# Optimization experiments

Hardware: AMD Instinct MI355X
Metric: run time of the kernel (lower is better)

The kernel has to match this reference:

```python
import jax, jax.numpy as jnp
import numpy as np

TOP_K = 2
B, T, D, H, E = 4, 2048, 1024, 2048, 8


def setup_inputs() -> dict:
    key = jax.random.key(0)
    ks = jax.random.split(key, 5)
    x = jax.random.normal(ks[0], (B, T, D), dtype=jnp.float32)
    # router: nn.Linear(dim, n_exp, bias=True) -> weight [E, D], bias [E]
    router_w = jax.random.normal(ks[1], (E, D), dtype=jnp.float32) * (D ** -0.5)
    router_b = jnp.zeros((E,), dtype=jnp.float32)
    # experts stacked: gate/up weight [E, H, D], down weight [E, D, H] (torch Linear is [out, in])
    w_gate = jax.random.normal(ks[2], (E, H, D), dtype=jnp.float32) * (D ** -0.5)
    w_up = jax.random.normal(ks[3], (E, H, D), dtype=jnp.float32) * (D ** -0.5)
    w_down = jax.random.normal(ks[4], (E, D, H), dtype=jnp.float32) * (H ** -0.5)
    return {"x": x, "router_w": router_w, "router_b": router_b,
            "w_gate": w_gate, "w_up": w_up, "w_down": w_down}


def reference(x, router_w, router_b, w_gate, w_up, w_down):
    b, t, d = x.shape
    n_exp = router_w.shape[0]
    flat = x.reshape(-1, d)                                  # [N, D]
    logits = flat @ router_w.T + router_b                    # [N, E]
    probs = jax.nn.softmax(logits, axis=-1)
    top_vals, top_idx = jax.lax.top_k(probs, TOP_K)          # [N, K]
    top_vals = top_vals / (jnp.sum(top_vals, axis=-1, keepdims=True) + 1e-9)
    # dense combine weights [N, E]: scatter normalized top-k probs to expert slots
    comb = jnp.sum(jax.nn.one_hot(top_idx, n_exp, dtype=flat.dtype) * top_vals[..., None], axis=1)
    # run every expert on every token (jit-friendly dense form of gather/scatter loop)
    g = jnp.einsum('nd,ehd->enh', flat, w_gate)              # [E, N, H]
    u = jnp.einsum('nd,ehd->enh', flat, w_up)
    h = jax.nn.silu(g) * u                                   # SwiGLU
    e_out = jnp.einsum('enh,edh->end', h, w_down)            # [E, N, D]
    out = jnp.einsum('ne,end->nd', comb, e_out)              # weighted combine
    return out.reshape(b, t, d)
```

## Files before the change

kernel.cpp:

```cpp
#include <hip/hip_runtime.h>
#include <hip/hip_bf16.h>
#include <stdint.h>


#define N_TOK 8192
#define D_DIM 1024
#define H_DIM 2048
#define N_EXP 8
#define N_ASSIGN (N_TOK * 2)
#define BM 128
#define BN 128
#define BK 64

typedef __attribute__((ext_vector_type(8))) short short8;
typedef __attribute__((ext_vector_type(4))) float f32x4;

__device__ __forceinline__ unsigned short f2bf(float f) {
  union { float f; unsigned int u; } v; v.f = f;
  unsigned int r = v.u + 0x7fffu + ((v.u >> 16) & 1u);
  return (unsigned short)(r >> 16);
}
__device__ __forceinline__ float bf2f(unsigned short u) {
  union { float f; unsigned int u; } v; v.u = ((unsigned int)u) << 16; return v.f;
}
__device__ __forceinline__ short8 pack8(float4 a, float4 b) {
  short8 o;
  o[0] = (short)f2bf(a.x); o[1] = (short)f2bf(a.y);
  o[2] = (short)f2bf(a.z); o[3] = (short)f2bf(a.w);
  o[4] = (short)f2bf(b.x); o[5] = (short)f2bf(b.y);
  o[6] = (short)f2bf(b.z); o[7] = (short)f2bf(b.w);
  return o;
}
__device__ __forceinline__ void gload_lds16(const void* g, void* l) {
  __builtin_amdgcn_global_load_lds((const __attribute__((address_space(1))) void*)g,
                                   (__attribute__((address_space(3))) void*)l, 16, 0, 0);
}

__global__ __launch_bounds__(256) void router_prep_kernel(
    const float* __restrict__ x, const float* __restrict__ rw,
    const float* __restrict__ rb,
    const float* __restrict__ wg, const float* __restrict__ wu,
    unsigned short* __restrict__ xb, unsigned short* __restrict__ wgu,
    int2* __restrict__ tiidx, float2* __restrict__ tiw) {
  int b = blockIdx.x;
  int tid = threadIdx.x;
  if (b >= 2048) {
    int idx = b - 2048;
    int up = idx >> 13;
    size_t i = (((size_t)(idx & 8191)) * 256 + tid) * 8;
    const float* src = up ? wu : wg;
    float4 a = *(const float4*)(src + i);
    float4 c = *(const float4*)(src + i + 4);
    int j = (int)(i >> 10);
    int e = j >> 11;
    int jj = j & (H_DIM - 1);
    int n = ((jj >> 4) << 5) + (up ? 16 : 0) + (jj & 15);
    size_t di = (((size_t)(e << 12) + n) << 10) + (i & 1023);
    *(short8*)(wgu + di) = pack8(a, c);
    return;
  }

  __shared__ float sw[N_EXP][D_DIM];
  for (int i = tid * 4; i < N_EXP * D_DIM; i += 1024)
    *(float4*)&sw[0][i] = *(const float4*)(rw + i);
  __syncthreads();

  int wave = tid >> 6, lane = tid & 63;
  int t = b * 4 + wave;
  const float2* xr = (const float2*)(x + (size_t)t * D_DIM);
  float2 xs[8];
#pragma unroll
  for (int j = 0; j < 8; j++) xs[j] = xr[lane + 64 * j];
  unsigned int* xbo = (unsigned int*)(xb + (size_t)t * D_DIM);
#pragma unroll
  for (int j = 0; j < 8; j++) {
    unsigned int pk = ((unsigned int)f2bf(xs[j].y) << 16) | (unsigned int)f2bf(xs[j].x);
    xbo[lane + 64 * j] = pk;
  }

  float logit[N_EXP];
#pragma unroll
  for (int e = 0; e < N_EXP; e++) {
    float acc = 0.f;
    const float2* swe = (const float2*)sw[e];
#pragma unroll
    for (int j = 0; j < 8; j++) {
      float2 w2 = swe[lane + 64 * j];
      acc += xs[j].x * w2.x + xs[j].y * w2.y;
    }
#pragma unroll
    for (int off = 32; off; off >>= 1) acc += __shfl_xor(acc, off);
    logit[e] = acc + rb[e];
  }
  if (lane == 0) {
    float m = logit[0];
#pragma unroll
    for (int e = 1; e < N_EXP; e++) m = fmaxf(m, logit[e]);
    float p[N_EXP], S = 0.f;
#pragma unroll
    for (int e = 0; e < N_EXP; e++) { p[e] = expf(logit[e] - m); S += p[e]; }
#pragma unroll
    for (int e = 0; e < N_EXP; e++) p[e] /= S;
    int i1 = 0; float v1 = p[0];
#pragma unroll
    for (int e = 1; e < N_EXP; e++) if (p[e] > v1) { v1 = p[e]; i1 = e; }
    int i2 = -1; float v2 = -1.f;
#pragma unroll
    for (int e = 0; e < N_EXP; e++) if (e != i1 && p[e] > v2) { v2 = p[e]; i2 = e; }
    float inv = 1.f / (v1 + v2 + 1e-9f);
    tiidx[t] = make_int2(i1, i2);
    tiw[t] = make_float2(v1 * inv, v2 * inv);
  }
}

__global__ __launch_bounds__(256) void plan_kernel(
    const int2* __restrict__ tiidx, int* __restrict__ cnt,
    int* __restrict__ off, int* __restrict__ assign, int2* __restrict__ trows) {
  __shared__ int sh[256][N_EXP + 1];
  __shared__ int soff[N_EXP];
  int tid = threadIdx.x;
  int t0 = tid * 32;

#pragma unroll
  for (int e = 0; e < N_EXP; e++) sh[tid][e] = 0;
  for (int i = 0; i < 32; i++) {
    int2 te = tiidx[t0 + i];
    sh[tid][te.x]++;
    sh[tid][te.y]++;
  }
  int oc[N_EXP];
#pragma unroll
  for (int e = 0; e < N_EXP; e++) oc[e] = sh[tid][e];
  __syncthreads();

  for (int s = 1; s < 256; s <<= 1) {
    int v[N_EXP];
#pragma unroll
    for (int e = 0; e < N_EXP; e++) v[e] = (tid >= s) ? sh[tid - s][e] : 0;
    __syncthreads();
#pragma unroll
    for (int e = 0; e < N_EXP; e++) sh[tid][e] += v[e];
    __syncthreads();
  }

  int ex[N_EXP];
#pragma unroll
  for (int e = 0; e < N_EXP; e++) ex[e] = sh[tid][e] - oc[e];
  if (tid == 0) {
    int a = 0;
    for (int e = 0; e < N_EXP; e++) {
      int tot = sh[255][e];
      soff[e] = a; off[e] = a; cnt[e] = tot; a += tot;
    }
    off[N_EXP] = a;
  }
  __syncthreads();
#pragma unroll
  for (int e = 0; e < N_EXP; e++) sh[tid][e] = ex[e];
  __syncthreads();

  for (int i = 0; i < 32; i++) {
    int t = t0 + i;
    int2 te = tiidx[t];
    int r1 = soff[te.x] + sh[tid][te.x]++;
    int r2 = soff[te.y] + sh[tid][te.y]++;
    assign[r1] = t;
    assign[r2] = t;
    trows[t] = make_int2(r1, r2);
  }
}

__global__ __launch_bounds__(256) void gemm_gateup(
    const unsigned short* __restrict__ xb,
    const unsigned short* __restrict__ wgu,
    const float* __restrict__ wd,
    unsigned short* __restrict__ wdb,
    const int* __restrict__ cnt, const int* __restrict__ off,
    const int* __restrict__ assign,
    unsigned short* __restrict__ hbuf) {
  int tid = threadIdx.x;
  if (blockIdx.z == 8) {
    size_t b0 = ((size_t)(blockIdx.x + 32 * blockIdx.y)) * 8192;
#pragma unroll
    for (int it = 0; it < 4; it++) {
      size_t i = b0 + ((size_t)it * 256 + tid) * 8;
      float4 a = *(const float4*)(wd + i);
      float4 c = *(const float4*)(wd + i + 4);
      *(short8*)(wdb + i) = pack8(a, c);
    }
    return;
  }
  int e = blockIdx.z;
  int nrows = cnt[e];
  int row0 = blockIdx.y * BM;
  if (row0 >= nrows) return;
  int col0 = blockIdx.x * BN;
  int base = off[e];

  __shared__ unsigned short sA[2][BM][BK];
  __shared__ unsigned short sB[2][BN][BK];

  int srow = tid >> 3;
  int dst8 = (tid & 7) * 8;
  int src8 = ((tid & 7) ^ (srow & 7)) * 8;

  const unsigned short* asrc[4];
  const unsigned short* bsrc[4];
#pragma unroll
  for (int i = 0; i < 4; i++) {
    int r = row0 + srow + 32 * i;
    int tok = (r < nrows) ? assign[base + r] : assign[base];
    asrc[i] = xb + (size_t)tok * D_DIM + src8;
    int wrow = (e << 12) + col0 + srow + 32 * i;
    bsrc[i] = wgu + (size_t)wrow * D_DIM + src8;
  }

  int wr = (tid >> 7) & 1, wc = (tid >> 6) & 1;
  int lane = tid & 63;
  int fr = lane & 15;
  int fk = (lane >> 4) * 8;
  int rx = (fr & 7) * 8;

  f32x4 acc[4][4];
#pragma unroll
  for (int a = 0; a < 4; a++)
#pragma unroll
    for (int b = 0; b < 4; b++) acc[a][b] = (f32x4){0.f, 0.f, 0.f, 0.f};

#define STAGE(bf, k0)                                                       \
  _Pragma("unroll")                                                         \
  for (int i = 0; i < 4; i++) {                                             \
    gload_lds16(asrc[i] + (k0), &sA[bf][srow + 32 * i][dst8]);              \
    gload_lds16(bsrc[i] + (k0), &sB[bf][srow + 32 * i][dst8]);              \
  }
#define COMPUTE(bf)                                                         \
  _Pragma("unroll")                                                         \
  for (int ks = 0; ks < 2; ks++) {                                          \
    short8 af[4], bq[4];                                                    \
    int c = (ks * 32 + fk) ^ rx;                                            \
    _Pragma("unroll")                                                       \
    for (int mb = 0; mb < 4; mb++)                                          \
      af[mb] = *(const short8*)&sA[bf][wr * 64 + mb * 16 + fr][c];          \
    _Pragma("unroll")                                                       \
    for (int nb = 0; nb < 4; nb++)                                          \
      bq[nb] = *(const short8*)&sB[bf][wc * 64 + nb * 16 + fr][c];          \
    _Pragma("unroll")                                                       \
    for (int mb = 0; mb < 4; mb++)                                          \
      _Pragma("unroll")                                                     \
      for (int nb = 0; nb < 4; nb++)                                        \
        acc[mb][nb] = __builtin_amdgcn_mfma_f32_16x16x32_bf16(              \
            af[mb], bq[nb], acc[mb][nb], 0, 0, 0);                          \
  }

  STAGE(0, 0);
  __syncthreads();
  for (int k0 = 0; k0 < D_DIM - 128; k0 += 128) {
    STAGE(1, k0 + 64);  COMPUTE(0); __syncthreads();
    STAGE(0, k0 + 128); COMPUTE(1); __syncthreads();
  }
  STAGE(1, D_DIM - 64); COMPUTE(0); __syncthreads();
  COMPUTE(1);
#undef STAGE
#undef COMPUTE

  int rowlim = nrows - row0;
#pragma unroll
  for (int mb = 0; mb < 4; mb++)
#pragma unroll
    for (int r = 0; r < 4; r++) {
      int lrow = wr * 64 + mb * 16 + (lane >> 4) * 4 + r;
      if (lrow < rowlim) {
        size_t hrow = (size_t)(base + row0 + lrow);
#pragma unroll
        for (int nbp = 0; nbp < 2; nbp++) {
          float g = acc[mb][2 * nbp][r], u = acc[mb][2 * nbp + 1][r];
          float hv = g / (1.f + __expf(-g)) * u;
          int hcol = (col0 >> 1) + wc * 32 + nbp * 16 + (lane & 15);
          hbuf[hrow * H_DIM + hcol] = f2bf(hv);
        }
      }
    }
}

__global__ __launch_bounds__(256) void gemm_down(
    const unsigned short* __restrict__ hbuf,
    const unsigned short* __restrict__ wd,
    const int* __restrict__ cnt, const int* __restrict__ off,
    unsigned short* __restrict__ eo) {
  int e = blockIdx.z;
  int nrows = cnt[e];
  int row0 = blockIdx.y * BM;
  if (row0 >= nrows) return;
  int col0 = blockIdx.x * BN;
  int base = off[e];

  __shared__ unsigned short sA[2][BM][BK];
  __shared__ unsigned short sB[2][BN][BK];

  int tid = threadIdx.x;
  int srow = tid >> 3;
  int dst8 = (tid & 7) * 8;
  int src8 = ((tid & 7) ^ (srow & 7)) * 8;

  const unsigned short* asrc[4];
  const unsigned short* bsrc[4];
#pragma unroll
  for (int i = 0; i < 4; i++) {
    int r = row0 + srow + 32 * i;
    int hrow = base + ((r < nrows) ? r : 0);
    asrc[i] = hbuf + (size_t)hrow * H_DIM + src8;
    int wrow = e * D_DIM + col0 + srow + 32 * i;
    bsrc[i] = wd + (size_t)wrow * H_DIM + src8;
  }

  int wr = (tid >> 7) & 1, wc = (tid >> 6) & 1;
  int lane = tid & 63;
  int fr = lane & 15;
  int fk = (lane >> 4) * 8;
  int rx = (fr & 7) * 8;

  f32x4 acc[4][4];
#pragma unroll
  for (int a = 0; a < 4; a++)
#pragma unroll
    for (int b = 0; b < 4; b++) acc[a][b] = (f32x4){0.f, 0.f, 0.f, 0.f};

#define STAGE(bf, k0)                                                       \
  _Pragma("unroll")                                                         \
  for (int i = 0; i < 4; i++) {                                             \
    gload_lds16(asrc[i] + (k0), &sA[bf][srow + 32 * i][dst8]);              \
    gload_lds16(bsrc[i] + (k0), &sB[bf][srow + 32 * i][dst8]);              \
  }
#define COMPUTE(bf)                                                         \
  _Pragma("unroll")                                                         \
  for (int ks = 0; ks < 2; ks++) {                                          \
    short8 af[4], bq[4];                                                    \
    int c = (ks * 32 + fk) ^ rx;                                            \
    _Pragma("unroll")                                                       \
    for (int mb = 0; mb < 4; mb++)                                          \
      af[mb] = *(const short8*)&sA[bf][wr * 64 + mb * 16 + fr][c];          \
    _Pragma("unroll")                                                       \
    for (int nb = 0; nb < 4; nb++)                                          \
      bq[nb] = *(const short8*)&sB[bf][wc * 64 + nb * 16 + fr][c];          \
    _Pragma("unroll")                                                       \
    for (int mb = 0; mb < 4; mb++)                                          \
      _Pragma("unroll")                                                     \
      for (int nb = 0; nb < 4; nb++)                                        \
        acc[mb][nb] = __builtin_amdgcn_mfma_f32_16x16x32_bf16(              \
            af[mb], bq[nb], acc[mb][nb], 0, 0, 0);                          \
  }

  STAGE(0, 0);
  __syncthreads();
  for (int k0 = 0; k0 < H_DIM - 128; k0 += 128) {
    STAGE(1, k0 + 64);  COMPUTE(0); __syncthreads();
    STAGE(0, k0 + 128); COMPUTE(1); __syncthreads();
  }
  STAGE(1, H_DIM - 64); COMPUTE(0); __syncthreads();
  COMPUTE(1);
#undef STAGE
#undef COMPUTE

  int rowlim = nrows - row0;
#pragma unroll
  for (int mb = 0; mb < 4; mb++)
#pragma unroll
    for (int r = 0; r < 4; r++) {
      int lrow = wr * 64 + mb * 16 + (lane >> 4) * 4 + r;
      if (lrow < rowlim) {
        size_t orow = (size_t)(base + row0 + lrow);
#pragma unroll
        for (int nb = 0; nb < 4; nb++)
          eo[orow * D_DIM + col0 + wc * 64 + nb * 16 + (lane & 15)] = f2bf(acc[mb][nb][r]);
      }
    }
}

__global__ __launch_bounds__(256) void combine_kernel(
    const unsigned short* __restrict__ eo, const int2* __restrict__ trows,
    const float2* __restrict__ tiw, float* __restrict__ out) {
  int t = blockIdx.x * 2 + (threadIdx.x >> 7);
  int l = threadIdx.x & 127;
  int c = l * 8;
  int2 r = trows[t];
  float2 w = tiw[t];
  short8 a = *(const short8*)&eo[(size_t)r.x * D_DIM + c];
  short8 b = *(const short8*)&eo[(size_t)r.y * D_DIM + c];
  float4 o0, o1;
  o0.x = w.x * bf2f((unsigned short)a[0]) + w.y * bf2f((unsigned short)b[0]);
  o0.y = w.x * bf2f((unsigned short)a[1]) + w.y * bf2f((unsigned short)b[1]);
  o0.z = w.x * bf2f((unsigned short)a[2]) + w.y * bf2f((unsigned short)b[2]);
  o0.w = w.x * bf2f((unsigned short)a[3]) + w.y * bf2f((unsigned short)b[3]);
  o1.x = w.x * bf2f((unsigned short)a[4]) + w.y * bf2f((unsigned short)b[4]);
  o1.y = w.x * bf2f((unsigned short)a[5]) + w.y * bf2f((unsigned short)b[5]);
  o1.z = w.x * bf2f((unsigned short)a[6]) + w.y * bf2f((unsigned short)b[6]);
  o1.w = w.x * bf2f((unsigned short)a[7]) + w.y * bf2f((unsigned short)b[7]);
  *(float4*)&out[(size_t)t * D_DIM + c] = o0;
  *(float4*)&out[(size_t)t * D_DIM + c + 4] = o1;
}

extern "C" void kernel_launch(void* const* d_in, const int* in_sizes, int n_in,
                              void* d_out, int out_size, void* d_ws, size_t ws_size,
                              hipStream_t stream) {
  const float* x  = (const float*)d_in[0];
  const float* rw = (const float*)d_in[1];
  const float* rb = (const float*)d_in[2];
  const float* wg = (const float*)d_in[3];
  const float* wu = (const float*)d_in[4];
  const float* wd = (const float*)d_in[5];
  float* out = (float*)d_out;

  char* ws = (char*)d_ws;
  size_t o = 0;
  auto alloc = [&](size_t b) { char* p = ws + o; o += (b + 255) & ~(size_t)255; return p; };
  unsigned short* xb  = (unsigned short*)alloc((size_t)N_TOK * D_DIM * 2);
  unsigned short* wgu = (unsigned short*)alloc((size_t)N_EXP * 4096 * D_DIM * 2);
  unsigned short* wdb = (unsigned short*)alloc((size_t)N_EXP * D_DIM * H_DIM * 2);
  unsigned short* hb  = (unsigned short*)alloc((size_t)N_ASSIGN * H_DIM * 2);
  unsigned short* eob = (unsigned short*)alloc((size_t)N_ASSIGN * D_DIM * 2);
  int*    assign = (int*)alloc(N_ASSIGN * 4);
  int2*   tiidx  = (int2*)alloc(N_TOK * 8);
  float2* tiw    = (float2*)alloc(N_TOK * 8);
  int2*   trows  = (int2*)alloc(N_TOK * 8);
  int*    cnt    = (int*)alloc(64);
  int*    off    = (int*)alloc(64);

  router_prep_kernel<<<2048 + 16384, 256, 0, stream>>>(
      x, rw, rb, wg, wu, xb, wgu, tiidx, tiw);
  plan_kernel<<<1, 256, 0, stream>>>(tiidx, cnt, off, assign, trows);
  gemm_gateup<<<dim3(4096 / BN, N_TOK / BM, N_EXP + 1), 256, 0, stream>>>(
      xb, wgu, wd, wdb, cnt, off, assign, hb);
  gemm_down<<<dim3(D_DIM / BN, N_TOK / BM, N_EXP), 256, 0, stream>>>(
      hb, wdb, cnt, off, eob);
  combine_kernel<<<N_TOK / 2, 256, 0, stream>>>(eob, trows, tiw, out);
}
```

Before: 352.5 us.

## Enlarge gate/up GEMM tile to 256x256 with 512 threads and tighter pipeline

```diff
diff --git a/kernel.cpp b/kernel.cpp
--- a/kernel.cpp
+++ b/kernel.cpp
@@ -170,7 +170,7 @@
   }
 }
 
-__global__ __launch_bounds__(256) void gemm_gateup(
+__global__ __launch_bounds__(512, 2) void gemm_gateup(
     const unsigned short* __restrict__ xb,
     const unsigned short* __restrict__ wgu,
     const float* __restrict__ wd,
@@ -180,10 +180,10 @@
     unsigned short* __restrict__ hbuf) {
   int tid = threadIdx.x;
   if (blockIdx.z == 8) {
-    size_t b0 = ((size_t)(blockIdx.x + 32 * blockIdx.y)) * 8192;
-#pragma unroll
-    for (int it = 0; it < 4; it++) {
-      size_t i = b0 + ((size_t)it * 256 + tid) * 8;
+    size_t b0 = ((size_t)(blockIdx.x + 16 * blockIdx.y)) * 4096;
+#pragma unroll
+    for (int it = 0; it < 8; it++) {
+      size_t i = (b0 + (size_t)it * 512 + tid) * 8;
       float4 a = *(const float4*)(wd + i);
       float4 c = *(const float4*)(wd + i + 4);
       *(short8*)(wdb + i) = pack8(a, c);
@@ -192,13 +192,13 @@
   }
   int e = blockIdx.z;
   int nrows = cnt[e];
-  int row0 = blockIdx.y * BM;
+  int row0 = blockIdx.y * 256;
   if (row0 >= nrows) return;
-  int col0 = blockIdx.x * BN;
+  int col0 = blockIdx.x * 256;
   int base = off[e];
 
-  __shared__ unsigned short sA[2][BM][BK];
-  __shared__ unsigned short sB[2][BN][BK];
+  __shared__ unsigned short sA[2][256][BK];
+  __shared__ unsigned short sB[2][256][BK];
 
   int srow = tid >> 3;
   int dst8 = (tid & 7) * 8;
@@ -208,44 +208,47 @@
   const unsigned short* bsrc[4];
 #pragma unroll
   for (int i = 0; i < 4; i++) {
-    int r = row0 + srow + 32 * i;
+    int r = row0 + srow + 64 * i;
     int tok = (r < nrows) ? assign[base + r] : assign[base];
     asrc[i] = xb + (size_t)tok * D_DIM + src8;
-    int wrow = (e << 12) + col0 + srow + 32 * i;
+    int wrow = (e << 12) + col0 + srow + 64 * i;
     bsrc[i] = wgu + (size_t)wrow * D_DIM + src8;
   }
 
-  int wr = (tid >> 7) & 1, wc = (tid >> 6) & 1;
+  int wid = tid >> 6;
+  int wr = wid >> 2;
+  int wc = wid & 3;
   int lane = tid & 63;
   int fr = lane & 15;
-  int fk = (lane >> 4) * 8;
+  int fq = lane >> 4;
+  int fk = fq * 8;
   int rx = (fr & 7) * 8;
 
-  f32x4 acc[4][4];
-#pragma unroll
-  for (int a = 0; a < 4; a++)
+  f32x4 acc[8][4];
+#pragma unroll
+  for (int a = 0; a < 8; a++)
 #pragma unroll
     for (int b = 0; b < 4; b++) acc[a][b] = (f32x4){0.f, 0.f, 0.f, 0.f};
 
 #define STAGE(bf, k0)                                                       \
   _Pragma("unroll")                                                         \
   for (int i = 0; i < 4; i++) {                                             \
-    gload_lds16(asrc[i] + (k0), &sA[bf][srow + 32 * i][dst8]);              \
-    gload_lds16(bsrc[i] + (k0), &sB[bf][srow + 32 * i][dst8]);              \
+    gload_lds16(asrc[i] + (k0), &sA[bf][srow + 64 * i][dst8]);              \
+    gload_lds16(bsrc[i] + (k0), &sB[bf][srow + 64 * i][dst8]);              \
   }
 #define COMPUTE(bf)                                                         \
   _Pragma("unroll")                                                         \
   for (int ks = 0; ks < 2; ks++) {                                          \
-    short8 af[4], bq[4];                                                    \
+    short8 af[8], bq[4];                                                    \
     int c = (ks * 32 + fk) ^ rx;                                            \
     _Pragma("unroll")                                                       \
-    for (int mb = 0; mb < 4; mb++)                                          \
-      af[mb] = *(const short8*)&sA[bf][wr * 64 + mb * 16 + fr][c];          \
+    for (int mb = 0; mb < 8; mb++)                                          \
+      af[mb] = *(const short8*)&sA[bf][wr * 128 + mb * 16 + fr][c];         \
     _Pragma("unroll")                                                       \
     for (int nb = 0; nb < 4; nb++)                                          \
       bq[nb] = *(const short8*)&sB[bf][wc * 64 + nb * 16 + fr][c];          \
     _Pragma("unroll")                                                       \
-    for (int mb = 0; mb < 4; mb++)                                          \
+    for (int mb = 0; mb < 8; mb++)                                          \
       _Pragma("unroll")                                                     \
       for (int nb = 0; nb < 4; nb++)                                        \
         acc[mb][nb] = __builtin_amdgcn_mfma_f32_16x16x32_bf16(              \
@@ -253,29 +256,40 @@
   }
 
   STAGE(0, 0);
-  __syncthreads();
-  for (int k0 = 0; k0 < D_DIM - 128; k0 += 128) {
-    STAGE(1, k0 + 64);  COMPUTE(0); __syncthreads();
-    STAGE(0, k0 + 128); COMPUTE(1); __syncthreads();
-  }
-  STAGE(1, D_DIM - 64); COMPUTE(0); __syncthreads();
+  for (int t = 0; t < 15; ++t) {
+    STAGE((t + 1) & 1, (t + 1) * BK);
+    asm volatile("s_waitcnt vmcnt(8)" ::: "memory");
+    __builtin_amdgcn_sched_barrier(0);
+    __builtin_amdgcn_s_barrier();
+    __builtin_amdgcn_sched_barrier(0);
+    __builtin_amdgcn_s_setprio(1);
+    COMPUTE(t & 1);
+    __builtin_amdgcn_s_setprio(0);
+    __builtin_amdgcn_sched_barrier(0);
+    __builtin_amdgcn_s_barrier();
+    __builtin_amdgcn_sched_barrier(0);
+  }
+  asm volatile("s_waitcnt vmcnt(0)" ::: "memory");
+  __builtin_amdgcn_sched_barrier(0);
+  __builtin_amdgcn_s_barrier();
+  __builtin_amdgcn_sched_barrier(0);
   COMPUTE(1);
 #undef STAGE
 #undef COMPUTE
 
   int rowlim = nrows - row0;
 #pragma unroll
-  for (int mb = 0; mb < 4; mb++)
+  for (int mb = 0; mb < 8; mb++)
 #pragma unroll
     for (int r = 0; r < 4; r++) {
-      int lrow = wr * 64 + mb * 16 + (lane >> 4) * 4 + r;
+      int lrow = wr * 128 + mb * 16 + fq * 4 + r;
       if (lrow < rowlim) {
         size_t hrow = (size_t)(base + row0 + lrow);
 #pragma unroll
         for (int nbp = 0; nbp < 2; nbp++) {
           float g = acc[mb][2 * nbp][r], u = acc[mb][2 * nbp + 1][r];
           float hv = g / (1.f + __expf(-g)) * u;
-          int hcol = (col0 >> 1) + wc * 32 + nbp * 16 + (lane & 15);
+          int hcol = (col0 >> 1) + wc * 32 + nbp * 16 + fr;
           hbuf[hrow * H_DIM + hcol] = f2bf(hv);
         }
       }
@@ -428,7 +442,7 @@
   router_prep_kernel<<<2048 + 16384, 256, 0, stream>>>(
       x, rw, rb, wg, wu, xb, wgu, tiidx, tiw);
   plan_kernel<<<1, 256, 0, stream>>>(tiidx, cnt, off, assign, trows);
-  gemm_gateup<<<dim3(4096 / BN, N_TOK / BM, N_EXP + 1), 256, 0, stream>>>(
+  gemm_gateup<<<dim3(4096 / 256, 32, N_EXP + 1), 512, 0, stream>>>(
       xb, wgu, wd, wdb, cnt, off, assign, hb);
   gemm_down<<<dim3(D_DIM / BN, N_TOK / BM, N_EXP), 256, 0, stream>>>(
       hb, wdb, cnt, off, eob);
```

New measurement: 368.2 us. 1.04x slower.
